# Optimization experiments

Measured on AMD Instinct MI355X. Metric: run time of the kernel, lower is better.

The kernel has to match this reference:

```python
import jax, jax.numpy as jnp
import numpy as np

N_RAYS = 131072          # rays in batch (e.g., 512x256 tile)
N_SAMPLES = 4194304      # total occupied samples after occ-grid culling (~32/ray)
STEP = 5e-3              # render_step_size (from render_step_size_vals)


def setup_inputs() -> dict:
    key = jax.random.key(0)
    k1, k2, k3, k4 = jax.random.split(key, 4)
    # sorted ray indices, as produced by occGrid.sampling (packed, ascending)
    ray_indices = jnp.sort(jax.random.randint(k1, (N_SAMPLES,), 0, N_RAYS)).astype(jnp.int32)
    t_starts = jax.random.uniform(k2, (N_SAMPLES,), jnp.float32) * 4.0
    t_ends = t_starts + STEP
    sigmas = jax.random.uniform(k3, (N_SAMPLES,), jnp.float32) * 50.0  # raw densities (density_scale=1)
    hdr = jax.random.uniform(k4, (N_SAMPLES, 3), jnp.float32)          # per-sample HDR radiance
    return {"t_starts": t_starts, "t_ends": t_ends, "sigmas": sigmas,
            "hdr": hdr, "ray_indices": ray_indices, "n_rays": N_RAYS}


def _render_and_accumulate(t_starts, t_ends, sigmas, hdr, ray_indices, n_rays):
    S = t_starts.shape[0]
    dt = t_ends - t_starts
    sdt = sigmas * dt                              # sigma * delta_t per sample
    alphas = 1.0 - jnp.exp(-sdt)                   # per-sample alpha
    # exclusive per-ray cumsum of sdt: global exclusive cumsum minus value at segment lead
    excl = jnp.cumsum(sdt) - sdt                   # global exclusive cumsum
    flag = jnp.concatenate([jnp.ones((1,), bool), ray_indices[1:] != ray_indices[:-1]])
    # index of the lead (first) sample of each ray segment, propagated forward
    lead = jax.lax.associative_scan(jnp.maximum, jnp.where(flag, jnp.arange(S), 0))
    trans = jnp.exp(-(excl - excl[lead]))          # transmittance T_i within each ray
    weights = trans * alphas                       # render_weight_from_density
    # accumulate_along_rays (segment reduce); indices are sorted
    opac = jax.ops.segment_sum(weights, ray_indices, num_segments=n_rays,
                               indices_are_sorted=True)                      # [n_rays]
    hdr_acc = jax.ops.segment_sum(weights[:, None] * hdr, ray_indices,
                                  num_segments=n_rays, indices_are_sorted=True)  # [n_rays,3]
    return jnp.concatenate([opac[:, None], hdr_acc], axis=-1)  # [n_rays, 4] = (opacity, hdr)


def reference(t_starts, t_ends, sigmas, hdr, ray_indices, n_rays):
    return _render_and_accumulate(t_starts, t_ends, sigmas, hdr, ray_indices, n_rays)
```

## Files before the change

kernel.cpp:

```cpp
#include <hip/hip_runtime.h>


#define TPB 256
#define LDSF (256 * 17)

#define DPP0(SRC, CTRL, RMASK, BC) __int_as_float(__builtin_amdgcn_update_dpp( \
        0, __float_as_int(SRC), (CTRL), (RMASK), 0xf, (BC)))

#define IMAXD(V, CTRL, RMASK, BC) { \
    int _tmp = __builtin_amdgcn_update_dpp(0, (V), (CTRL), (RMASK), 0xf, (BC)); \
    (V) = ((V) > _tmp) ? (V) : _tmp; }

#define ADD4(A, B) make_float4((A).x + (B).x, (A).y + (B).y, (A).z + (B).z, (A).w + (B).w)

__device__ __forceinline__ float fold16_dpp(float x) {
    float a = 0.0f;
    a = __fadd_rn(a, DPP0(x, 0x110 | 15, 0xf, true));
    a = __fadd_rn(a, DPP0(x, 0x110 | 14, 0xf, true));
    a = __fadd_rn(a, DPP0(x, 0x110 | 13, 0xf, true));
    a = __fadd_rn(a, DPP0(x, 0x110 | 12, 0xf, true));
    a = __fadd_rn(a, DPP0(x, 0x110 | 11, 0xf, true));
    a = __fadd_rn(a, DPP0(x, 0x110 | 10, 0xf, true));
    a = __fadd_rn(a, DPP0(x, 0x110 |  9, 0xf, true));
    a = __fadd_rn(a, DPP0(x, 0x110 |  8, 0xf, true));
    a = __fadd_rn(a, DPP0(x, 0x110 |  7, 0xf, true));
    a = __fadd_rn(a, DPP0(x, 0x110 |  6, 0xf, true));
    a = __fadd_rn(a, DPP0(x, 0x110 |  5, 0xf, true));
    a = __fadd_rn(a, DPP0(x, 0x110 |  4, 0xf, true));
    a = __fadd_rn(a, DPP0(x, 0x110 |  3, 0xf, true));
    a = __fadd_rn(a, DPP0(x, 0x110 |  2, 0xf, true));
    a = __fadd_rn(a, DPP0(x, 0x110 |  1, 0xf, true));
    a = __fadd_rn(a, x);
    return a;
}

__device__ __forceinline__ float wscan(float v) {
    v = __fadd_rn(v, DPP0(v, 0x111, 0xf, true));
    v = __fadd_rn(v, DPP0(v, 0x112, 0xf, true));
    v = __fadd_rn(v, DPP0(v, 0x114, 0xf, true));
    v = __fadd_rn(v, DPP0(v, 0x118, 0xf, true));
    v = __fadd_rn(v, DPP0(v, 0x142, 0xa, false));
    v = __fadd_rn(v, DPP0(v, 0x143, 0xc, false));
    return v;
}

__device__ __forceinline__ float sdt_c(float tsv, float tev, float sgv) {
    return __fmul_rn(sgv, __fsub_rn(tev, tsv));
}

__global__ void k_bottom(const float* __restrict__ ts, const float* __restrict__ te,
                         const float* __restrict__ sg, int S,
                         float* __restrict__ sdt, float* __restrict__ s1,
                         float* __restrict__ T1,
                         float4* __restrict__ out4, int n_rays) {
    __shared__ float lds[LDSF];
    int t = threadIdx.x;
    int tile = blockIdx.x;
    int gid = tile * TPB + t;
    if (gid < n_rays) out4[gid] = make_float4(0.f, 0.f, 0.f, 0.f);
    const float4* ts4 = (const float4*)ts;
    const float4* te4 = (const float4*)te;
    const float4* sg4 = (const float4*)sg;
    float4* sdt4 = (float4*)sdt;
    #pragma unroll
    for (int k = 0; k < 4; ++k) {
        int idx4 = tile * 1024 + k * 256 + t;
        float4 a = ts4[idx4], b = te4[idx4], c = sg4[idx4];
        float4 xo;
        xo.x = sdt_c(a.x, b.x, c.x);
        xo.y = sdt_c(a.y, b.y, c.y);
        xo.z = sdt_c(a.z, b.z, c.z);
        xo.w = sdt_c(a.w, b.w, c.w);
        sdt4[idx4] = xo;
        int fl = (k * 256 + t) << 2;
        int g0 = fl >> 4, j0 = fl & 15;
        float* p = &lds[g0 * 17 + j0];
        p[0] = xo.x; p[1] = xo.y; p[2] = xo.z; p[3] = xo.w;
    }
    __syncthreads();
    float acc = 0.0f;
    #pragma unroll
    for (int j = 0; j < 16; ++j) acc = __fadd_rn(acc, lds[t * 17 + j]);
    float acc2 = fold16_dpp(acc);
    int g = tile * 256 + t;
    s1[g] = acc2;
    if ((t & 15) == 15) T1[g >> 4] = acc2;
}

__global__ void k_mid(const float* __restrict__ T1, float* __restrict__ C2) {
    __shared__ float T2sh[1024];
    __shared__ float s3sh[1024];
    __shared__ float s4sh[64];
    __shared__ float T3sh[64];
    __shared__ float T4sh[4];
    __shared__ float C5sh[4];
    int t = threadIdx.x;
    const float4* T14 = (const float4*)T1;
    float s2l[16];
    float acc = 0.0f;
    #pragma unroll
    for (int k = 0; k < 4; ++k) {
        float4 v = T14[t * 4 + k];
        acc = __fadd_rn(acc, v.x); s2l[k * 4 + 0] = acc;
        acc = __fadd_rn(acc, v.y); s2l[k * 4 + 1] = acc;
        acc = __fadd_rn(acc, v.z); s2l[k * 4 + 2] = acc;
        acc = __fadd_rn(acc, v.w); s2l[k * 4 + 3] = acc;
    }
    T2sh[t] = acc;
    __syncthreads();
    if (t < 64) {
        float a3 = 0.0f;
        for (int j = 0; j < 16; ++j) { a3 = __fadd_rn(a3, T2sh[t * 16 + j]); s3sh[t * 16 + j] = a3; }
        T3sh[t] = a3;
    }
    __syncthreads();
    if (t < 4) {
        float a4 = 0.0f;
        for (int j = 0; j < 16; ++j) { a4 = __fadd_rn(a4, T3sh[t * 16 + j]); s4sh[t * 16 + j] = a4; }
        T4sh[t] = a4;
    }
    __syncthreads();
    if (t == 0) {
        float c = 0.0f;
        for (int r = 0; r < 4; ++r) { c = __fadd_rn(c, T4sh[r]); C5sh[r] = c; }
    }
    __syncthreads();
    if (t < 64) {
        int r = t >> 4;
        float v4 = s4sh[t];
        s4sh[t] = r ? __fadd_rn(v4, C5sh[r - 1]) : v4;
    }
    __syncthreads();
    {
        int r = t >> 4;
        float v3 = s3sh[t];
        float c3 = r ? __fadd_rn(v3, s4sh[r - 1]) : v3;
        s3sh[t] = c3;
    }
    __syncthreads();
    float c3m = t ? s3sh[t - 1] : 0.0f;
    float4* C24 = (float4*)C2;
    #pragma unroll
    for (int k = 0; k < 4; ++k) {
        float4 o;
        o.x = t ? __fadd_rn(s2l[k * 4 + 0], c3m) : s2l[k * 4 + 0];
        o.y = t ? __fadd_rn(s2l[k * 4 + 1], c3m) : s2l[k * 4 + 1];
        o.z = t ? __fadd_rn(s2l[k * 4 + 2], c3m) : s2l[k * 4 + 2];
        o.w = t ? __fadd_rn(s2l[k * 4 + 3], c3m) : s2l[k * 4 + 3];
        C24[t * 4 + k] = o;
    }
}

__global__ void k_render(const int* __restrict__ ri, const float* __restrict__ sdt,
                         const float* __restrict__ s1, const float* __restrict__ C2,
                         const float* __restrict__ hdr,
                         int S, float* __restrict__ out) {
    const int tid = blockIdx.x * TPB + threadIdx.x;
    const int t = threadIdx.x & 63;
    const int i0 = tid * 8;
    const bool valid = i0 < S;

    float4 xa, xb; int4 ra, rb;
    if (valid) {
        xa = ((const float4*)sdt)[2 * tid];
        xb = ((const float4*)sdt)[2 * tid + 1];
        ra = ((const int4*)ri)[2 * tid];
        rb = ((const int4*)ri)[2 * tid + 1];
    } else {
        xa = xb = make_float4(0.f, 0.f, 0.f, 0.f);
        ra.x = ra.y = ra.z = ra.w = -1 - t;
        rb = ra;
    }

    int dpr = __builtin_amdgcn_update_dpp(0, rb.w, 0x111, 0xf, 0xf, true);
    int prev_r = dpr;
    if ((t & 15) == 0) prev_r = (i0 == 0 || !valid) ? (ra.x ^ 1) : ri[i0 - 1];

    bool f0 = prev_r != ra.x;
    bool f1 = ra.y != ra.x, f2 = ra.z != ra.y, f3 = ra.w != ra.z;
    bool f4 = rb.x != ra.w, f5 = rb.y != rb.x, f6 = rb.z != rb.y, f7 = rb.w != rb.z;
    unsigned long long mask0 = __ballot(f0);

    float p0 = __fadd_rn(0.0f, xa.x);
    float p1 = __fadd_rn(p0, xa.y);
    float p2 = __fadd_rn(p1, xa.z);
    float p3 = __fadd_rn(p2, xa.w);
    float p4 = __fadd_rn(p3, xb.x);
    float p5 = __fadd_rn(p4, xb.y);
    float p6 = __fadd_rn(p5, xb.z);
    float p7 = __fadd_rn(p6, xb.w);
    {
        float cin = DPP0(p7, 0x111, 0xf, true);
        float n0 = __fadd_rn(cin, xa.x);
        float n1 = __fadd_rn(n0, xa.y);
        float n2 = __fadd_rn(n1, xa.z);
        float n3 = __fadd_rn(n2, xa.w);
        float n4 = __fadd_rn(n3, xb.x);
        float n5 = __fadd_rn(n4, xb.y);
        float n6 = __fadd_rn(n5, xb.z);
        float n7 = __fadd_rn(n6, xb.w);
        bool me = (t & 1) != 0;
        p0 = me ? n0 : p0; p1 = me ? n1 : p1;
        p2 = me ? n2 : p2; p3 = me ? n3 : p3;
        p4 = me ? n4 : p4; p5 = me ? n5 : p5;
        p6 = me ? n6 : p6; p7 = me ? n7 : p7;
    }

    int g = i0 >> 4;
    float cj = 0.0f;
    if (valid && g) {
        int j3 = g - 1;
        cj = (j3 >> 4) ? __fadd_rn(s1[j3], C2[(j3 >> 4) - 1]) : s1[j3];
    }
    float e0 = __fsub_rn(g ? __fadd_rn(p0, cj) : p0, xa.x);
    float e1 = __fsub_rn(g ? __fadd_rn(p1, cj) : p1, xa.y);
    float e2 = __fsub_rn(g ? __fadd_rn(p2, cj) : p2, xa.z);
    float e3 = __fsub_rn(g ? __fadd_rn(p3, cj) : p3, xa.w);
    float e4 = __fsub_rn(g ? __fadd_rn(p4, cj) : p4, xb.x);
    float e5 = __fsub_rn(g ? __fadd_rn(p5, cj) : p5, xb.y);
    float e6 = __fsub_rn(g ? __fadd_rn(p6, cj) : p6, xb.z);
    float e7 = __fsub_rn(g ? __fadd_rn(p7, cj) : p7, xb.w);

    float el_lead = 0.0f;
    if (!(mask0 & 1ull)) {
        int wbs = (tid - t) * 8;
        int r0v = __builtin_amdgcn_readfirstlane(ra.x);
        int h0 = 0;
        for (int round = 0; round < 65536; ++round) {
            int idx = wbs - 1 - t - 64 * round;
            int rv = (idx >= 0) ? ri[idx] : (r0v ^ 1);
            unsigned long long mm = __ballot(rv != r0v);
            if (mm) {
                int lm = __ffsll((unsigned long long)mm) - 1;
                h0 = wbs - 64 * round - lm;
                break;
            }
        }
        float elv = 0.0f;
        if (t == 0) {
            const float4* s4 = (const float4*)sdt;
            int gh = h0 >> 4, lh = h0 & 15;
            float4 q0 = s4[gh * 4 + 0], q1 = s4[gh * 4 + 1];
            float4 q2 = s4[gh * 4 + 2], q3 = s4[gh * 4 + 3];
            float vv[16] = { q0.x, q0.y, q0.z, q0.w, q1.x, q1.y, q1.z, q1.w,
                             q2.x, q2.y, q2.z, q2.w, q3.x, q3.y, q3.z, q3.w };
            float a2 = 0.0f, xl = 0.0f;
            #pragma unroll
            for (int j2 = 0; j2 < 16; ++j2) {
                if (j2 <= lh) { a2 = __fadd_rn(a2, vv[j2]); xl = vv[j2]; }
            }
            float Ch = a2;
            if (gh) {
                int j3b = gh - 1;
                float cjb = (j3b >> 4) ? __fadd_rn(s1[j3b], C2[(j3b >> 4) - 1]) : s1[j3b];
                Ch = __fadd_rn(a2, cjb);
            }
            elv = __fsub_rn(Ch, xl);
        }
        el_lead = __int_as_float(__builtin_amdgcn_readfirstlane(__float_as_int(elv)));
    }

    bool hb0 = f0, hb1 = f1 | hb0, hb2 = f2 | hb1, hb3 = f3 | hb2;
    bool hb4 = f4 | hb3, hb5 = f5 | hb4, hb6 = f6 | hb5, hb7 = f7 | hb6;

    int key = (valid && hb7) ? (t + 1) : 0;
    int sk = __shfl_up(key, 1, 64);
    if (t == 0) sk = 0;
    int M = sk;
    IMAXD(M, 0x111, 0xf, true)
    IMAXD(M, 0x112, 0xf, true)
    IMAXD(M, 0x114, 0xf, true)
    IMAXD(M, 0x118, 0xf, true)
    IMAXD(M, 0x142, 0xa, false)
    IMAXD(M, 0x143, 0xc, false)
    int src = M;
    int psrc = (src > 0) ? (src - 1) : t;

    float el7c = f7 ? e7 : f6 ? e6 : f5 ? e5 : f4 ? e4 :
                 f3 ? e3 : f2 ? e2 : f1 ? e1 : f0 ? e0 : 0.0f;
    float rel = __shfl(el7c, psrc, 64);
    float el_prev = (src > 0) ? rel : el_lead;

    float el0 = f0 ? e0 : el_prev;
    float el1 = f1 ? e1 : el0;
    float el2 = f2 ? e2 : el1;
    float el3 = f3 ? e3 : el2;
    float el4 = f4 ? e4 : el3;
    float el5 = f5 ? e5 : el4;
    float el6 = f6 ? e6 : el5;
    float el7 = f7 ? e7 : el6;

    float4 h0v, h1v, h2v, h3v, h4v, h5v;
    if (valid) {
        const float4* h4 = (const float4*)hdr;
        h0v = h4[6 * tid + 0]; h1v = h4[6 * tid + 1]; h2v = h4[6 * tid + 2];
        h3v = h4[6 * tid + 3]; h4v = h4[6 * tid + 4]; h5v = h4[6 * tid + 5];
    } else {
        h0v = h1v = h2v = h3v = h4v = h5v = make_float4(0.f, 0.f, 0.f, 0.f);
    }
    float w0 = 0.f, w1 = 0.f, w2 = 0.f, w3 = 0.f;
    float w4 = 0.f, w5 = 0.f, w6 = 0.f, w7 = 0.f;
    if (valid) {
        w0 = __fmul_rn(__expf(-__fsub_rn(e0, el0)), __fsub_rn(1.0f, __expf(-xa.x)));
        w1 = __fmul_rn(__expf(-__fsub_rn(e1, el1)), __fsub_rn(1.0f, __expf(-xa.y)));
        w2 = __fmul_rn(__expf(-__fsub_rn(e2, el2)), __fsub_rn(1.0f, __expf(-xa.z)));
        w3 = __fmul_rn(__expf(-__fsub_rn(e3, el3)), __fsub_rn(1.0f, __expf(-xa.w)));
        w4 = __fmul_rn(__expf(-__fsub_rn(e4, el4)), __fsub_rn(1.0f, __expf(-xb.x)));
        w5 = __fmul_rn(__expf(-__fsub_rn(e5, el5)), __fsub_rn(1.0f, __expf(-xb.y)));
        w6 = __fmul_rn(__expf(-__fsub_rn(e6, el6)), __fsub_rn(1.0f, __expf(-xb.z)));
        w7 = __fmul_rn(__expf(-__fsub_rn(e7, el7)), __fsub_rn(1.0f, __expf(-xb.w)));
    }
    float4 v0 = make_float4(w0, __fmul_rn(w0, h0v.x), __fmul_rn(w0, h0v.y), __fmul_rn(w0, h0v.z));
    float4 v1 = make_float4(w1, __fmul_rn(w1, h0v.w), __fmul_rn(w1, h1v.x), __fmul_rn(w1, h1v.y));
    float4 v2 = make_float4(w2, __fmul_rn(w2, h1v.z), __fmul_rn(w2, h1v.w), __fmul_rn(w2, h2v.x));
    float4 v3 = make_float4(w3, __fmul_rn(w3, h2v.y), __fmul_rn(w3, h2v.z), __fmul_rn(w3, h2v.w));
    float4 v4 = make_float4(w4, __fmul_rn(w4, h3v.x), __fmul_rn(w4, h3v.y), __fmul_rn(w4, h3v.z));
    float4 v5 = make_float4(w5, __fmul_rn(w5, h3v.w), __fmul_rn(w5, h4v.x), __fmul_rn(w5, h4v.y));
    float4 v6 = make_float4(w6, __fmul_rn(w6, h4v.z), __fmul_rn(w6, h4v.w), __fmul_rn(w6, h5v.x));
    float4 v7 = make_float4(w7, __fmul_rn(w7, h5v.y), __fmul_rn(w7, h5v.z), __fmul_rn(w7, h5v.w));

    float4 V0 = v0;
    float4 V1 = ADD4(V0, v1);
    float4 V2 = ADD4(V1, v2);
    float4 V3 = ADD4(V2, v3);
    float4 V4 = ADD4(V3, v4);
    float4 V5 = ADD4(V4, v5);
    float4 V6 = ADD4(V5, v6);
    float4 V7 = ADD4(V6, v7);

    float4 W;
    W.x = wscan(V7.x); W.y = wscan(V7.y); W.z = wscan(V7.z); W.w = wscan(V7.w);
    float4 E;
    E.x = __shfl_up(W.x, 1, 64);
    E.y = __shfl_up(W.y, 1, 64);
    E.z = __shfl_up(W.z, 1, 64);
    E.w = __shfl_up(W.w, 1, 64);
    if (t == 0) { E.x = 0.f; E.y = 0.f; E.z = 0.f; E.w = 0.f; }

    float4 Z = make_float4(0.f, 0.f, 0.f, 0.f);
    float4 B0 = f0 ? E : Z;
    float4 B1 = f1 ? ADD4(E, V0) : B0;
    float4 B2 = f2 ? ADD4(E, V1) : B1;
    float4 B3 = f3 ? ADD4(E, V2) : B2;
    float4 B4 = f4 ? ADD4(E, V3) : B3;
    float4 B5 = f5 ? ADD4(E, V4) : B4;
    float4 B6 = f6 ? ADD4(E, V5) : B5;
    float4 B7 = f7 ? ADD4(E, V6) : B6;

    float4 rbs;
    rbs.x = __shfl(B7.x, psrc, 64);
    rbs.y = __shfl(B7.y, psrc, 64);
    rbs.z = __shfl(B7.z, psrc, 64);
    rbs.w = __shfl(B7.w, psrc, 64);
    float4 bs_prev = (src > 0) ? rbs : Z;

    bool tl0 = f1, tl1 = f2, tl2 = f3, tl3 = f4, tl4 = f5, tl5 = f6, tl6 = f7;
    bool tl7 = (t < 63) ? (((mask0 >> (t + 1)) & 1ull) != 0ull) : true;
    bool rt7 = (t < 63);

#define EMIT(K, TLK, RJ, VK, RT) \
    if (valid && (TLK) && (RJ) >= 0) { \
        float4 bse = hb##K ? B##K : bs_prev; \
        float px = (E.x + (VK).x) - bse.x; \
        float py = (E.y + (VK).y) - bse.y; \
        float pz = (E.z + (VK).z) - bse.z; \
        float pw = (E.w + (VK).w) - bse.w; \
        float* o = out + 4 * (RJ); \
        bool priv = (hb##K || (src > 0)) && (RT); \
        if (priv) { \
            *(float4*)o = make_float4(px, py, pz, pw); \
        } else { \
            atomicAdd(o + 0, px); \
            atomicAdd(o + 1, py); \
            atomicAdd(o + 2, pz); \
            atomicAdd(o + 3, pw); \
        } \
    }
    EMIT(0, tl0, ra.x, V0, true)
    EMIT(1, tl1, ra.y, V1, true)
    EMIT(2, tl2, ra.z, V2, true)
    EMIT(3, tl3, ra.w, V3, true)
    EMIT(4, tl4, rb.x, V4, true)
    EMIT(5, tl5, rb.y, V5, true)
    EMIT(6, tl6, rb.z, V6, true)
    EMIT(7, tl7, rb.w, V7, rt7)
#undef EMIT
}

extern "C" void kernel_launch(void* const* d_in, const int* in_sizes, int n_in,
                              void* d_out, int out_size, void* d_ws, size_t ws_size,
                              hipStream_t stream) {
    const float* ts  = (const float*)d_in[0];
    const float* te  = (const float*)d_in[1];
    const float* sg  = (const float*)d_in[2];
    const float* hdr = (const float*)d_in[3];
    const int*   ri  = (const int*)d_in[4];
    const int S      = in_sizes[0];
    const int n_rays = out_size / 4;
    const int N1 = S >> 4;
    const int N2 = N1 >> 4;

    char* w = (char*)d_ws;
    auto alloc = [&](size_t bytes) { char* p = w; w += (bytes + 255) & ~255ULL; return p; };
    float* sdt = (float*)alloc((size_t)S * 4);
    float* s1  = (float*)alloc((size_t)N1 * 4);
    float* T1  = (float*)alloc((size_t)N2 * 4);
    float* C2  = (float*)alloc((size_t)N2 * 4);

    k_bottom<<<dim3(N1 / TPB), dim3(TPB), 0, stream>>>(ts, te, sg, S, sdt, s1, T1,
                                                       (float4*)d_out, n_rays);
    k_mid   <<<dim3(1), dim3(1024), 0, stream>>>(T1, C2);
    k_render<<<dim3(S / (TPB * 8)), dim3(TPB), 0, stream>>>(ri, sdt, s1, C2, hdr,
                                                            S, (float*)d_out);
}
```

Baseline: 165.7 us.

## Fold mid-level scan kernel into render kernel, recomputing top prefixes per block

Removes the single-block k_mid launch and instead has every k_render block redundantly reduce the 16K-entry T1 array into shared-memory prefix sums, then build the few C2 carries it needs. This eliminates one kernel launch and a serial single-block stage between the bottom and render kernels. In exchange, each of the 2048 render blocks reads all of T1 and runs several syncthreads-separated scan phases before its main work, which adds redundant global traffic and latency per block. Lead-lookups that fall outside the block's window recompute the carry from T1 on the fly.

```diff
diff --git a/kernel.cpp b/kernel.cpp
--- a/kernel.cpp
+++ b/kernel.cpp
@@ -87,74 +87,84 @@
     if ((t & 15) == 15) T1[g >> 4] = acc2;
 }
 
-__global__ void k_mid(const float* __restrict__ T1, float* __restrict__ C2) {
+__global__ void k_render(const int* __restrict__ ri, const float* __restrict__ sdt,
+                         const float* __restrict__ s1, const float* __restrict__ T1,
+                         const float* __restrict__ hdr,
+                         int S, float* __restrict__ out) {
     __shared__ float T2sh[1024];
     __shared__ float s3sh[1024];
     __shared__ float s4sh[64];
     __shared__ float T3sh[64];
     __shared__ float T4sh[4];
     __shared__ float C5sh[4];
-    int t = threadIdx.x;
+    __shared__ float C2nd[10];
+    const int tx = threadIdx.x;
     const float4* T14 = (const float4*)T1;
-    float s2l[16];
-    float acc = 0.0f;
+
     #pragma unroll
-    for (int k = 0; k < 4; ++k) {
-        float4 v = T14[t * 4 + k];
-        acc = __fadd_rn(acc, v.x); s2l[k * 4 + 0] = acc;
-        acc = __fadd_rn(acc, v.y); s2l[k * 4 + 1] = acc;
-        acc = __fadd_rn(acc, v.z); s2l[k * 4 + 2] = acc;
-        acc = __fadd_rn(acc, v.w); s2l[k * 4 + 3] = acc;
-    }
-    T2sh[t] = acc;
-    __syncthreads();
-    if (t < 64) {
+    for (int q = 0; q < 4; ++q) {
+        int grp = tx + 256 * q;
+        float a2 = 0.0f;
+        #pragma unroll
+        for (int kk = 0; kk < 4; ++kk) {
+            float4 v = T14[grp * 4 + kk];
+            a2 = __fadd_rn(a2, v.x);
+            a2 = __fadd_rn(a2, v.y);
+            a2 = __fadd_rn(a2, v.z);
+            a2 = __fadd_rn(a2, v.w);
+        }
+        T2sh[grp] = a2;
+    }
+    __syncthreads();
+    if (tx < 64) {
         float a3 = 0.0f;
-        for (int j = 0; j < 16; ++j) { a3 = __fadd_rn(a3, T2sh[t * 16 + j]); s3sh[t * 16 + j] = a3; }
-        T3sh[t] = a3;
-    }
-    __syncthreads();
-    if (t < 4) {
+        for (int j = 0; j < 16; ++j) { a3 = __fadd_rn(a3, T2sh[tx * 16 + j]); s3sh[tx * 16 + j] = a3; }
+        T3sh[tx] = a3;
+    }
+    __syncthreads();
+    if (tx < 4) {
         float a4 = 0.0f;
-        for (int j = 0; j < 16; ++j) { a4 = __fadd_rn(a4, T3sh[t * 16 + j]); s4sh[t * 16 + j] = a4; }
-        T4sh[t] = a4;
-    }
-    __syncthreads();
-    if (t == 0) {
+        for (int j = 0; j < 16; ++j) { a4 = __fadd_rn(a4, T3sh[tx * 16 + j]); s4sh[tx * 16 + j] = a4; }
+        T4sh[tx] = a4;
+    }
+    __syncthreads();
+    if (tx == 0) {
         float c = 0.0f;
         for (int r = 0; r < 4; ++r) { c = __fadd_rn(c, T4sh[r]); C5sh[r] = c; }
     }
     __syncthreads();
-    if (t < 64) {
-        int r = t >> 4;
-        float v4 = s4sh[t];
-        s4sh[t] = r ? __fadd_rn(v4, C5sh[r - 1]) : v4;
-    }
-    __syncthreads();
-    {
-        int r = t >> 4;
-        float v3 = s3sh[t];
-        float c3 = r ? __fadd_rn(v3, s4sh[r - 1]) : v3;
-        s3sh[t] = c3;
-    }
-    __syncthreads();
-    float c3m = t ? s3sh[t - 1] : 0.0f;
-    float4* C24 = (float4*)C2;
-    #pragma unroll
-    for (int k = 0; k < 4; ++k) {
-        float4 o;
-        o.x = t ? __fadd_rn(s2l[k * 4 + 0], c3m) : s2l[k * 4 + 0];
-        o.y = t ? __fadd_rn(s2l[k * 4 + 1], c3m) : s2l[k * 4 + 1];
-        o.z = t ? __fadd_rn(s2l[k * 4 + 2], c3m) : s2l[k * 4 + 2];
-        o.w = t ? __fadd_rn(s2l[k * 4 + 3], c3m) : s2l[k * 4 + 3];
-        C24[t * 4 + k] = o;
-    }
-}
-
-__global__ void k_render(const int* __restrict__ ri, const float* __restrict__ sdt,
-                         const float* __restrict__ s1, const float* __restrict__ C2,
-                         const float* __restrict__ hdr,
-                         int S, float* __restrict__ out) {
+    if (tx < 64) {
+        int r = tx >> 4;
+        float v4 = s4sh[tx];
+        s4sh[tx] = r ? __fadd_rn(v4, C5sh[r - 1]) : v4;
+    }
+    __syncthreads();
+    for (int e = tx; e < 1024; e += 256) {
+        int r = e >> 4;
+        float v3 = s3sh[e];
+        s3sh[e] = r ? __fadd_rn(v3, s4sh[r - 1]) : v3;
+    }
+    __syncthreads();
+    if (tx < 10) {
+        int m = blockIdx.x * 8 - 2 + tx;
+        float c2v = 0.0f;
+        if (m >= 0) {
+            int grp = m >> 4, lm = m & 15;
+            float4 q0 = T14[grp * 4 + 0], q1 = T14[grp * 4 + 1];
+            float4 q2 = T14[grp * 4 + 2], q3 = T14[grp * 4 + 3];
+            float vv[16] = { q0.x, q0.y, q0.z, q0.w, q1.x, q1.y, q1.z, q1.w,
+                             q2.x, q2.y, q2.z, q2.w, q3.x, q3.y, q3.z, q3.w };
+            float a2 = 0.0f;
+            #pragma unroll
+            for (int j2 = 0; j2 < 16; ++j2) {
+                if (j2 <= lm) a2 = __fadd_rn(a2, vv[j2]);
+            }
+            c2v = grp ? __fadd_rn(a2, s3sh[grp - 1]) : a2;
+        }
+        C2nd[tx] = c2v;
+    }
+    __syncthreads();
+
     const int tid = blockIdx.x * TPB + threadIdx.x;
     const int t = threadIdx.x & 63;
     const int i0 = tid * 8;
@@ -210,7 +220,8 @@
     float cj = 0.0f;
     if (valid && g) {
         int j3 = g - 1;
-        cj = (j3 >> 4) ? __fadd_rn(s1[j3], C2[(j3 >> 4) - 1]) : s1[j3];
+        int m4 = j3 >> 4;
+        cj = m4 ? __fadd_rn(s1[j3], C2nd[m4 + 1 - blockIdx.x * 8]) : s1[j3];
     }
     float e0 = __fsub_rn(g ? __fadd_rn(p0, cj) : p0, xa.x);
     float e1 = __fsub_rn(g ? __fadd_rn(p1, cj) : p1, xa.y);
@@ -252,7 +263,25 @@
             float Ch = a2;
             if (gh) {
                 int j3b = gh - 1;
-                float cjb = (j3b >> 4) ? __fadd_rn(s1[j3b], C2[(j3b >> 4) - 1]) : s1[j3b];
+                int mb = j3b >> 4;
+                float cjb;
+                if (mb) {
+                    int m = mb - 1;
+                    int grp2 = m >> 4, lm2 = m & 15;
+                    float4 u0 = T14[grp2 * 4 + 0], u1 = T14[grp2 * 4 + 1];
+                    float4 u2 = T14[grp2 * 4 + 2], u3 = T14[grp2 * 4 + 3];
+                    float uu[16] = { u0.x, u0.y, u0.z, u0.w, u1.x, u1.y, u1.z, u1.w,
+                                     u2.x, u2.y, u2.z, u2.w, u3.x, u3.y, u3.z, u3.w };
+                    float s2v = 0.0f;
+                    #pragma unroll
+                    for (int j2 = 0; j2 < 16; ++j2) {
+                        if (j2 <= lm2) s2v = __fadd_rn(s2v, uu[j2]);
+                    }
+                    float c2v = grp2 ? __fadd_rn(s2v, s3sh[grp2 - 1]) : s2v;
+                    cjb = __fadd_rn(s1[j3b], c2v);
+                } else {
+                    cjb = s1[j3b];
+                }
                 Ch = __fadd_rn(a2, cjb);
             }
             elv = __fsub_rn(Ch, xl);
@@ -405,11 +434,9 @@
     float* sdt = (float*)alloc((size_t)S * 4);
     float* s1  = (float*)alloc((size_t)N1 * 4);
     float* T1  = (float*)alloc((size_t)N2 * 4);
-    float* C2  = (float*)alloc((size_t)N2 * 4);
 
     k_bottom<<<dim3(N1 / TPB), dim3(TPB), 0, stream>>>(ts, te, sg, S, sdt, s1, T1,
                                                        (float4*)d_out, n_rays);
-    k_mid   <<<dim3(1), dim3(1024), 0, stream>>>(T1, C2);
-    k_render<<<dim3(S / (TPB * 8)), dim3(TPB), 0, stream>>>(ri, sdt, s1, C2, hdr,
+    k_render<<<dim3(S / (TPB * 8)), dim3(TPB), 0, stream>>>(ri, sdt, s1, T1, hdr,
                                                             S, (float*)d_out);
 }
```

New measurement: 170.8 us. 3.1% more time.
